# Performance work log

Hardware: AMD Instinct MI355X
Metric: run time of the kernel (lower is better)

The kernel has to match this reference:

```python
import jax, jax.numpy as jnp
import numpy as np

B, S, D = 2, 2048, 2048
H, HKV = 32, 8
HD = D // H  # 64
NEG_INF = -1e9


def _rope_tables(seq_len, head_dim):
    inv_freq = 1.0 / (10000.0 ** (np.arange(0, head_dim, 2, dtype=np.float32) / head_dim))
    t = np.arange(seq_len, dtype=np.float32)
    freqs = np.outer(t, inv_freq)                      # (S, HD/2)
    emb = np.concatenate([freqs, freqs], axis=-1)      # (S, HD)
    cos = np.cos(emb)[None, None]                      # (1,1,S,HD)
    sin = np.sin(emb)[None, None]
    return jnp.asarray(cos), jnp.asarray(sin)


def setup_inputs() -> dict:
    key = jax.random.key(0)
    ks = jax.random.split(key, 5)
    hidden_states = jax.random.normal(ks[0], (B, S, D), dtype=jnp.float32)
    # causal additive mask: 0 where allowed, -inf (large negative) where masked
    causal = jnp.tril(jnp.ones((S, S), dtype=jnp.bool_))
    attention_mask = jnp.where(causal, 0.0, NEG_INF).astype(jnp.float32)
    attention_mask = jnp.broadcast_to(attention_mask[None, None], (B, 1, S, S))
    cos, sin = _rope_tables(S, HD)
    sc = 0.02
    Wq = jax.random.normal(ks[1], (D, H * HD), dtype=jnp.float32) * sc
    Wk = jax.random.normal(ks[2], (D, HKV * HD), dtype=jnp.float32) * sc
    Wv = jax.random.normal(ks[3], (D, HKV * HD), dtype=jnp.float32) * sc
    Wo = jax.random.normal(ks[4], (H * HD, D), dtype=jnp.float32) * sc
    return {"hidden_states": hidden_states, "attention_mask": attention_mask,
            "cos": cos, "sin": sin, "Wq": Wq, "Wk": Wk, "Wv": Wv, "Wo": Wo}


def _rotate_half(x):
    x1, x2 = jnp.split(x, 2, axis=-1)
    return jnp.concatenate([-x2, x1], axis=-1)


def _apply_rope(x, cos, sin):
    # x: (B, h, S, HD); cos/sin: (1,1,S,HD)
    return x * cos + _rotate_half(x) * sin


def reference(hidden_states, attention_mask, cos, sin, Wq, Wk, Wv, Wo):
    b, s, _ = hidden_states.shape
    scale = 1.0 / np.sqrt(HD)
    q = (hidden_states @ Wq).reshape(b, s, H, HD).transpose(0, 2, 1, 3)    # (B,H,S,HD)
    k = (hidden_states @ Wk).reshape(b, s, HKV, HD).transpose(0, 2, 1, 3)  # (B,HKV,S,HD)
    v = (hidden_states @ Wv).reshape(b, s, HKV, HD).transpose(0, 2, 1, 3)
    q = _apply_rope(q, cos, sin)
    k = _apply_rope(k, cos, sin)
    # GQA: group query heads per kv head without materializing repeated KV
    g = H // HKV
    qg = q.reshape(b, HKV, g, s, HD)
    scores = jnp.einsum('bkgqd,bksd->bkgqs', qg, k) * scale               # (B,HKV,g,S,S)
    scores = scores + attention_mask[:, :, None]                          # broadcast (B,1,1,S,S)
    attn = jax.nn.softmax(scores, axis=-1)
    out = jnp.einsum('bkgqs,bksd->bkgqd', attn, v)                        # (B,HKV,g,S,HD)
    out = out.reshape(b, H, s, HD).transpose(0, 2, 1, 3).reshape(b, s, H * HD)
    return out @ Wo
```

## Files before the change

kernel.cpp:

```cpp
#include <hip/hip_runtime.h>
#include <math.h>

typedef _Float16 half8 __attribute__((ext_vector_type(8)));
typedef _Float16 half4 __attribute__((ext_vector_type(4)));
typedef _Float16 half2 __attribute__((ext_vector_type(2)));
typedef float f32x4 __attribute__((ext_vector_type(4)));

#define S_LEN 2048
#define DM    2048
#define NH    32
#define NKV   8

#define QSCALE 0.1803368801111204f
#define NSHIFT -11.541560327111707f

#if __has_builtin(__builtin_amdgcn_exp2f)
#define EXP2(x) __builtin_amdgcn_exp2f(x)
#else
#define EXP2(x) __builtin_exp2f(x)
#endif

__device__ __forceinline__ half2 pkrtz(float a, float b) {
    return __builtin_bit_cast(half2, __builtin_amdgcn_cvt_pkrtz(a, b));
}

__device__ __forceinline__ void async16(const void* g, void* l) {
    __builtin_amdgcn_global_load_lds(
        (const __attribute__((address_space(1))) unsigned int*)g,
        (__attribute__((address_space(3))) unsigned int*)l, 16, 0, 0);
}

__global__ __launch_bounds__(256) void cast_h(const float* __restrict__ x,
                                              _Float16* __restrict__ y, int n)
{
    int i = (blockIdx.x * 256 + threadIdx.x) * 4;
    if (i >= n) return;
    float4 v = *(const float4*)(x + i);
    half4 o = {(_Float16)v.x, (_Float16)v.y, (_Float16)v.z, (_Float16)v.w};
    *(half4*)(y + i) = o;
}

__global__ __launch_bounds__(256) void transpose_all(
    const float* __restrict__ Wq, const float* __restrict__ Wk,
    const float* __restrict__ Wv, const float* __restrict__ Wo,
    _Float16* __restrict__ Wqkv_t, _Float16* __restrict__ Wo_t)
{
    const int z = blockIdx.z;
    const float* W; _Float16* Wt; int N;
    if (z == 0)      { W = Wq; Wt = Wqkv_t;                        N = 2048; }
    else if (z == 1) { W = Wk; Wt = Wqkv_t + (size_t)2048 * 2048;  N = 512;  }
    else if (z == 2) { W = Wv; Wt = Wqkv_t + (size_t)2560 * 2048;  N = 512;  }
    else             { W = Wo; Wt = Wo_t;                          N = 2048; }
    if ((int)blockIdx.x * 32 >= N) return;

    __shared__ float t[32][33];
    const int n0 = blockIdx.x * 32, k0 = blockIdx.y * 32;
    const int tx = threadIdx.x & 31, ty = threadIdx.x >> 5;
#pragma unroll
    for (int i = 0; i < 32; i += 8)
        t[ty + i][tx] = W[(size_t)(k0 + ty + i) * N + n0 + tx];
    __syncthreads();
#pragma unroll
    for (int i = 0; i < 32; i += 8)
        Wt[(size_t)(n0 + ty + i) * 2048 + k0 + tx] = (_Float16)t[tx][ty + i];
}

__global__ __launch_bounds__(512, 2) void gemm_h(
    const _Float16* __restrict__ A, const _Float16* __restrict__ Bt,
    void* __restrict__ Cout, int N, int K, int mode,
    const float* __restrict__ cosT, const float* __restrict__ sinT)
{
    __shared__ __align__(16) _Float16 Lds[2][4][8192];
    const int tid  = threadIdx.x;
    const int lane = tid & 63;
    const int wave = tid >> 6;
    const int lm = lane & 15, quad = lane >> 4;
    const int wm = wave >> 2;
    const int wn = wave & 3;

    const int gx  = gridDim.x;
    const int nwg = gx * gridDim.y;
    const int lin = blockIdx.y * gx + blockIdx.x;
    const int tsw = (lin & 7) * (nwg >> 3) + (lin >> 3);
    const int bm  = (tsw / gx) * 256, bn = (tsw % gx) * 256;
    const int nt  = K >> 6;

    const int sr   = tid >> 3;
    const int lg   = (tid & 7) ^ (sr & 7);
    const int grow = sr * 2 + (lg >> 2);
    const int gcol = (lg & 3) << 3;
    const _Float16* pA0 = A  + (size_t)(bm + grow) * K + gcol;
    const _Float16* pB0 = Bt + (size_t)(bn + grow) * K + gcol;
    char* ldsb = (char*)Lds + tid * 16;

#define STAGE(t, idx) do { if ((t) < nt) {                          \
        const int koff_ = (t) * 64 + (((idx) >> 1) << 5);           \
        const _Float16* s_ = (((idx) & 1) ? pA0 : pB0) + koff_;     \
        char* d_ = ldsb + (((t) & 1) << 16) + ((idx) << 14);        \
        async16(s_, d_);                                            \
        async16(s_ + (size_t)128 * K, d_ + 8192);                   \
    } } while (0)

    const int chsw = (((((lm & 1) << 2) | quad) ^ (lm >> 1)) << 3);
    const int ar = (wm << 6) + (lm >> 1);
    const int br = (wn << 5) + (lm >> 1);
    const _Float16* Lh = (const _Float16*)Lds;

    f32x4 acc[8][4];
#pragma unroll
    for (int i = 0; i < 8; ++i)
#pragma unroll
        for (int j = 0; j < 4; ++j) acc[i][j] = (f32x4){0.f, 0.f, 0.f, 0.f};

    STAGE(0, 0); STAGE(0, 1); STAGE(0, 2); STAGE(0, 3);
    STAGE(1, 0); STAGE(1, 1); STAGE(1, 2);
    if (nt > 1) asm volatile("s_waitcnt vmcnt(6)" ::: "memory");
    else        asm volatile("s_waitcnt vmcnt(0)" ::: "memory");
    __builtin_amdgcn_s_barrier();

    half8 af[4], bf[4];
#define MFMA16(mb)                                                            \
    _Pragma("unroll") for (int i_ = 0; i_ < 4; ++i_)                          \
    _Pragma("unroll") for (int j_ = 0; j_ < 4; ++j_)                          \
        acc[(mb) + i_][j_] = __builtin_amdgcn_mfma_f32_16x16x32_f16(          \
            af[i_], bf[j_], acc[(mb) + i_][j_], 0, 0, 0);

#define PH_BAR()  __builtin_amdgcn_s_barrier();                               \
                  asm volatile("s_waitcnt lgkmcnt(0)" ::: "memory");          \
                  __builtin_amdgcn_s_setprio(1)
#define PH_END()  __builtin_amdgcn_s_setprio(0);                              \
                  __builtin_amdgcn_s_barrier()

    int p = 0;
    for (int G = 0; G < nt; ++G, p ^= 1) {
        const _Float16* Lp = Lh + (p << 15);
        const _Float16* Au0 = Lp + 8192  + ar * 64 + chsw;
        const _Float16* Au1 = Lp + 24576 + ar * 64 + chsw;
        const _Float16* Bu0 = Lp +         br * 64 + chsw;
        const _Float16* Bu1 = Lp + 16384 + br * 64 + chsw;
#pragma unroll
        for (int i = 0; i < 4; ++i) af[i] = *(const half8*)(Au0 + i * 512);
#pragma unroll
        for (int j = 0; j < 4; ++j) bf[j] = *(const half8*)(Bu0 + j * 512);
        STAGE(G + 1, 3);
        PH_BAR(); MFMA16(0); PH_END();
#pragma unroll
        for (int i = 0; i < 4; ++i) af[i] = *(const half8*)(Au0 + 2048 + i * 512);
        STAGE(G + 2, 0);
        PH_BAR(); MFMA16(4); PH_END();
#pragma unroll
        for (int i = 0; i < 4; ++i) af[i] = *(const half8*)(Au1 + i * 512);
#pragma unroll
        for (int j = 0; j < 4; ++j) bf[j] = *(const half8*)(Bu1 + j * 512);
        STAGE(G + 2, 1);
        PH_BAR(); MFMA16(0); PH_END();
#pragma unroll
        for (int i = 0; i < 4; ++i) af[i] = *(const half8*)(Au1 + 2048 + i * 512);
        STAGE(G + 2, 2);
        PH_BAR(); MFMA16(4);
        __builtin_amdgcn_s_setprio(0);
        if (G + 2 < nt) asm volatile("s_waitcnt vmcnt(6)" ::: "memory");
        else            asm volatile("s_waitcnt vmcnt(0)" ::: "memory");
        __builtin_amdgcn_s_barrier();
    }
#undef STAGE
#undef MFMA16
#undef PH_BAR
#undef PH_END

    const int mrowq = bm + (wm << 7) + (quad << 2);
    if (mode == 0) {
        float* C = (float*)Cout;
        const int col0 = bn + (wn << 6) + lm;
#pragma unroll
        for (int mf = 0; mf < 8; ++mf)
#pragma unroll
            for (int r = 0; r < 4; ++r) {
                const int m = mrowq + mf * 16 + r;
#pragma unroll
                for (int nf = 0; nf < 4; ++nf)
                    C[(size_t)m * N + col0 + nf * 16] = acc[mf][nf][r];
            }
        return;
    }

    _Float16* Cq = (_Float16*)Cout;
    _Float16* Ck = Cq + (size_t)2 * NH * S_LEN * 64;
    _Float16* Cv = Ck + (size_t)2 * NKV * S_LEN * 64;
    const int colbase = bn + (wn << 6);
    const int region = (colbase >= 2560) ? 2 : (colbase >= 2048) ? 1 : 0;

    if (region == 2) {
        const int head = (colbase - 2560) >> 6;
#pragma unroll
        for (int mf = 0; mf < 8; ++mf) {
            const int m0 = mrowq + mf * 16;
            const int b = m0 >> 11, s0 = m0 & 2047;
#pragma unroll
            for (int nf = 0; nf < 4; ++nf) {
                half2 lo = pkrtz(acc[mf][nf][0], acc[mf][nf][1]);
                half2 hi = pkrtz(acc[mf][nf][2], acc[mf][nf][3]);
                half4 ov = {lo[0], lo[1], hi[0], hi[1]};
                *(half4*)(Cv + ((((size_t)b * NKV + head) << 6) + lm + nf * 16) * S_LEN + s0) = ov;
            }
        }
        return;
    }

    const float qscale = (region == 0) ? QSCALE : 1.0f;
    const int head = (region == 0) ? (colbase >> 6) : ((colbase - 2048) >> 6);
    _Float16* Cdst = (region == 0) ? Cq : Ck;
    const int nh = (region == 0) ? NH : NKV;
#pragma unroll
    for (int mf = 0; mf < 8; ++mf)
#pragma unroll
        for (int r = 0; r < 4; ++r) {
            int m = mrowq + mf * 16 + r;
            int b = m >> 11, s = m & 2047;
            const float c0 = cosT[s * 64 + lm], c16 = cosT[s * 64 + lm + 16];
            const float s0 = sinT[s * 64 + lm], s16 = sinT[s * 64 + lm + 16];
            float a0r = acc[mf][0][r], a1r = acc[mf][1][r];
            float a2r = acc[mf][2][r], a3r = acc[mf][3][r];
            float o0 = (a0r * c0  - a2r * s0)  * qscale;
            float o1 = (a1r * c16 - a3r * s16) * qscale;
            float o2 = (a2r * c0  + a0r * s0)  * qscale;
            float o3 = (a3r * c16 + a1r * s16) * qscale;
            _Float16* d = Cdst + ((((size_t)b * nh + head) * S_LEN + s) << 6) + lm;
            d[0]  = (_Float16)o0;
            d[16] = (_Float16)o1;
            d[32] = (_Float16)o2;
            d[48] = (_Float16)o3;
        }
}

#define LSWOFS(row, halfofs) \
    ((row) * 64 + (((((halfofs) >> 3) & 7) ^ ((row) & 7)) << 3) + ((halfofs) & 7))

__global__ __launch_bounds__(256, 2) void attn_h(
    const _Float16* __restrict__ q, const _Float16* __restrict__ k,
    const _Float16* __restrict__ vt, _Float16* __restrict__ x2)
{
    __shared__ __align__(16) _Float16 Ks[2][64 * 64];
    __shared__ __align__(16) _Float16 Vts[2][64 * 64];

    const int kvh = blockIdx.y, b = blockIdx.z;
    const int tid = threadIdx.x;
    const int wave = tid >> 6, lane = tid & 63;
    const int lm = lane & 15, quad = lane >> 4;
    const int h = kvh * 4 + wave;

    const int qtT[2] = {63 - (int)blockIdx.x, (int)blockIdx.x};
    const int ktm[2] = {(qtT[0] * 32 + 31) >> 6, (qtT[1] * 32 + 31) >> 6};

    const _Float16* kbase  = k  + ((((size_t)b * NKV + kvh) * S_LEN) << 6);
    const _Float16* vtbase = vt + ((((size_t)b * NKV + kvh) << 6) * S_LEN);

    half8 qf[2][2][2];
#pragma unroll
    for (int tp = 0; tp < 2; ++tp) {
        const _Float16* qb = q + ((((size_t)b * NH + h) * S_LEN + qtT[tp] * 32) << 6);
#pragma unroll
        for (int i = 0; i < 2; ++i)
#pragma unroll
            for (int kk = 0; kk < 2; ++kk)
                qf[tp][i][kk] = *(const half8*)(qb + (i * 16 + lm) * 64 + kk * 32 + quad * 8);
    }

    f32x4 accOT[2][2][4];
    float lpart[2][2];
#pragma unroll
    for (int tp = 0; tp < 2; ++tp)
#pragma unroll
        for (int i = 0; i < 2; ++i) {
            lpart[tp][i] = 0.f;
#pragma unroll
            for (int j = 0; j < 4; ++j) accOT[tp][i][j] = (f32x4){0.f, 0.f, 0.f, 0.f};
        }

    const int f0 = tid * 16, f1 = 4096 + tid * 16;
    const int r0 = f0 >> 7, r1 = f1 >> 7;
    const int c0 = ((f0 >> 4) & 7) ^ (r0 & 7);
    const int c1 = ((f1 >> 4) & 7) ^ (r1 & 7);
    const char* ksrc0 = (const char*)kbase  + r0 * 128 + c0 * 16;
    const char* ksrc1 = (const char*)kbase  + r1 * 128 + c1 * 16;
    const char* vsrc0 = (const char*)vtbase + (size_t)r0 * 4096 + c0 * 16;
    const char* vsrc1 = (const char*)vtbase + (size_t)r1 * 4096 + c1 * 16;

#define STAGEKV(kt, nb) do {                                          \
        async16(ksrc0 + (size_t)(kt) * 8192, (char*)Ks[nb]  + f0);    \
        async16(ksrc1 + (size_t)(kt) * 8192, (char*)Ks[nb]  + f1);    \
        async16(vsrc0 + (kt) * 128,          (char*)Vts[nb] + f0);    \
        async16(vsrc1 + (kt) * 128,          (char*)Vts[nb] + f1);    \
    } while (0)

    STAGEKV(0, 0);
    asm volatile("s_waitcnt vmcnt(0)" ::: "memory");
    __builtin_amdgcn_s_barrier();

    for (int kt = 0; kt <= ktm[0]; ++kt) {
        const int cur = kt & 1;
        if (kt < ktm[0]) STAGEKV(kt + 1, cur ^ 1);
        const _Float16* Kc = Ks[cur];
        const _Float16* Vc = Vts[cur];

        half8 kf[4][2];
        half4 vtf[4][4];
#pragma unroll
        for (int t = 0; t < 4; ++t) {
#pragma unroll
            for (int kk = 0; kk < 2; ++kk)
                kf[t][kk] = *(const half8*)(Kc + LSWOFS(t * 16 + lm, kk * 32 + quad * 8));
#pragma unroll
            for (int j = 0; j < 4; ++j)
                vtf[j][t] = *(const half4*)(Vc + LSWOFS(j * 16 + lm, t * 16 + quad * 4));
        }

#pragma unroll
        for (int tp = 0; tp < 2; ++tp) {
            if (kt > ktm[tp]) continue;
            const bool diag = (kt == ktm[tp]);
#pragma unroll
            for (int i = 0; i < 2; ++i) {
                f32x4 sc[4];
                __builtin_amdgcn_s_setprio(1);
#pragma unroll
                for (int t = 0; t < 4; ++t) {
                    f32x4 z = (f32x4){NSHIFT, NSHIFT, NSHIFT, NSHIFT};
                    z = __builtin_amdgcn_mfma_f32_16x16x32_f16(kf[t][0], qf[tp][i][0], z, 0, 0, 0);
                    z = __builtin_amdgcn_mfma_f32_16x16x32_f16(kf[t][1], qf[tp][i][1], z, 0, 0, 0);
                    sc[t] = z;
                }
                __builtin_amdgcn_s_setprio(0);
                if (diag) {
                    const int qpos = qtT[tp] * 32 + i * 16 + lm;
#pragma unroll
                    for (int t = 0; t < 4; ++t)
#pragma unroll
                        for (int r = 0; r < 4; ++r) {
                            int key = kt * 64 + t * 16 + quad * 4 + r;
                            if (key > qpos) sc[t][r] = -30000.f;
                        }
                }
                half4 pt[4];
                float lp = 0.f;
#pragma unroll
                for (int t = 0; t < 4; ++t) {
                    float p0 = EXP2(sc[t][0]), p1 = EXP2(sc[t][1]);
                    float p2 = EXP2(sc[t][2]), p3 = EXP2(sc[t][3]);
                    lp += (p0 + p1) + (p2 + p3);
                    half2 lo = pkrtz(p0, p1);
                    half2 hi = pkrtz(p2, p3);
                    pt[t] = (half4){lo[0], lo[1], hi[0], hi[1]};
                }
                lpart[tp][i] += lp;
                __builtin_amdgcn_s_setprio(1);
#pragma unroll
                for (int j = 0; j < 4; ++j)
#pragma unroll
                    for (int t = 0; t < 4; ++t)
                        accOT[tp][i][j] = __builtin_amdgcn_mfma_f32_16x16x16f16(
                            vtf[j][t], pt[t], accOT[tp][i][j], 0, 0, 0);
                __builtin_amdgcn_s_setprio(0);
            }
        }
        asm volatile("s_waitcnt vmcnt(0)" ::: "memory");
        __builtin_amdgcn_s_barrier();
    }
#undef STAGEKV

#pragma unroll
    for (int tp = 0; tp < 2; ++tp)
#pragma unroll
        for (int i = 0; i < 2; ++i) {
            float l = lpart[tp][i];
            l += __shfl_xor(l, 16);
            l += __shfl_xor(l, 32);
            const float inv = 1.f / l;
            const size_t row = (size_t)b * S_LEN + qtT[tp] * 32 + i * 16 + lm;
#pragma unroll
            for (int j = 0; j < 4; ++j) {
                f32x4 o = accOT[tp][i][j];
                half2 lo = pkrtz(o[0] * inv, o[1] * inv);
                half2 hi = pkrtz(o[2] * inv, o[3] * inv);
                half4 ov = {lo[0], lo[1], hi[0], hi[1]};
                *(half4*)(x2 + row * DM + h * 64 + j * 16 + quad * 4) = ov;
            }
        }
}

extern "C" void kernel_launch(void* const* d_in, const int* in_sizes, int n_in,
                              void* d_out, int out_size, void* d_ws, size_t ws_size,
                              hipStream_t stream)
{
    const float* hidden = (const float*)d_in[0];
    const float* cosT = (const float*)d_in[2];
    const float* sinT = (const float*)d_in[3];
    const float* Wq = (const float*)d_in[4];
    const float* Wk = (const float*)d_in[5];
    const float* Wv = (const float*)d_in[6];
    const float* Wo = (const float*)d_in[7];
    float* out = (float*)d_out;

    _Float16* w = (_Float16*)d_ws;
    _Float16* hid_h  = w;  w += (size_t)4096 * 2048;
    _Float16* Wqkv_t = w;  w += (size_t)3072 * 2048;
    _Float16* Wo_t   = w;  w += (size_t)2048 * 2048;
    _Float16* qh     = w;  w += (size_t)2 * NH * S_LEN * 64;
    _Float16* kh     = w;  w += (size_t)2 * NKV * S_LEN * 64;
    _Float16* vth    = w;  w += (size_t)2 * NKV * S_LEN * 64;
    _Float16* x2h    = w;

    dim3 blk(256);
    cast_h<<<dim3(8192), blk, 0, stream>>>(hidden, hid_h, 8388608);
    transpose_all<<<dim3(64, 64, 4), blk, 0, stream>>>(Wq, Wk, Wv, Wo, Wqkv_t, Wo_t);

    gemm_h<<<dim3(12, 16), dim3(512), 0, stream>>>(hid_h, Wqkv_t, qh, 3072, 2048, 1, cosT, sinT);

    attn_h<<<dim3(32, 8, 2), blk, 0, stream>>>(qh, kh, vth, x2h);

    gemm_h<<<dim3(8, 16), dim3(512), 0, stream>>>(x2h, Wo_t, out, 2048, 2048, 0, nullptr, nullptr);
}
```

Measured before the change: 323.1 us.

## Merge input cast into transpose kernel and restructure GEMM pipeline into two half-phases

Folds the hidden-state fp32-to-fp16 cast into the weight transpose kernel as an extra grid z-slice, removing one kernel launch. The GEMM main loop changes from four quarter-phases with a two-tile prefetch to two half-phases that each load eight A fragments and issue 32 MFMAs, prefetching only one tile ahead. This cuts the barrier count per K-step but shortens the lookahead on global loads and raises register pressure from the larger A fragment array.

```diff
diff --git a/kernel.cpp b/kernel.cpp
--- a/kernel.cpp
+++ b/kernel.cpp
@@ -30,22 +30,23 @@
         (__attribute__((address_space(3))) unsigned int*)l, 16, 0, 0);
 }
 
-__global__ __launch_bounds__(256) void cast_h(const float* __restrict__ x,
-                                              _Float16* __restrict__ y, int n)
-{
-    int i = (blockIdx.x * 256 + threadIdx.x) * 4;
-    if (i >= n) return;
-    float4 v = *(const float4*)(x + i);
-    half4 o = {(_Float16)v.x, (_Float16)v.y, (_Float16)v.z, (_Float16)v.w};
-    *(half4*)(y + i) = o;
-}
-
-__global__ __launch_bounds__(256) void transpose_all(
+__global__ __launch_bounds__(256) void prep_all(
     const float* __restrict__ Wq, const float* __restrict__ Wk,
     const float* __restrict__ Wv, const float* __restrict__ Wo,
-    _Float16* __restrict__ Wqkv_t, _Float16* __restrict__ Wo_t)
+    const float* __restrict__ hidden,
+    _Float16* __restrict__ Wqkv_t, _Float16* __restrict__ Wo_t,
+    _Float16* __restrict__ hid_h)
 {
     const int z = blockIdx.z;
+    if (z == 4) {
+        const size_t i = ((size_t)(blockIdx.y * 64 + blockIdx.x) * 256 + threadIdx.x) * 8;
+        float4 v0 = *(const float4*)(hidden + i);
+        float4 v1 = *(const float4*)(hidden + i + 4);
+        half8 o = {(_Float16)v0.x, (_Float16)v0.y, (_Float16)v0.z, (_Float16)v0.w,
+                   (_Float16)v1.x, (_Float16)v1.y, (_Float16)v1.z, (_Float16)v1.w};
+        *(half8*)(hid_h + i) = o;
+        return;
+    }
     const float* W; _Float16* Wt; int N;
     if (z == 0)      { W = Wq; Wt = Wqkv_t;                        N = 2048; }
     else if (z == 1) { W = Wk; Wt = Wqkv_t + (size_t)2048 * 2048;  N = 512;  }
@@ -113,23 +114,22 @@
         for (int j = 0; j < 4; ++j) acc[i][j] = (f32x4){0.f, 0.f, 0.f, 0.f};
 
     STAGE(0, 0); STAGE(0, 1); STAGE(0, 2); STAGE(0, 3);
-    STAGE(1, 0); STAGE(1, 1); STAGE(1, 2);
-    if (nt > 1) asm volatile("s_waitcnt vmcnt(6)" ::: "memory");
+    if (nt > 1) asm volatile("s_waitcnt vmcnt(4)" ::: "memory");
     else        asm volatile("s_waitcnt vmcnt(0)" ::: "memory");
     __builtin_amdgcn_s_barrier();
 
-    half8 af[4], bf[4];
-#define MFMA16(mb)                                                            \
-    _Pragma("unroll") for (int i_ = 0; i_ < 4; ++i_)                          \
+    half8 af[8], bf[4];
+#define MFMA32()                                                              \
+    _Pragma("unroll") for (int i_ = 0; i_ < 8; ++i_)                          \
     _Pragma("unroll") for (int j_ = 0; j_ < 4; ++j_)                          \
-        acc[(mb) + i_][j_] = __builtin_amdgcn_mfma_f32_16x16x32_f16(          \
-            af[i_], bf[j_], acc[(mb) + i_][j_], 0, 0, 0);
-
-#define PH_BAR()  __builtin_amdgcn_s_barrier();                               \
-                  asm volatile("s_waitcnt lgkmcnt(0)" ::: "memory");          \
-                  __builtin_amdgcn_s_setprio(1)
-#define PH_END()  __builtin_amdgcn_s_setprio(0);                              \
-                  __builtin_amdgcn_s_barrier()
+        acc[i_][j_] = __builtin_amdgcn_mfma_f32_16x16x32_f16(                 \
+            af[i_], bf[j_], acc[i_][j_], 0, 0, 0);
+
+#define PH_TAIL(cond)                                                         \
+    __builtin_amdgcn_s_setprio(0);                                            \
+    if (cond) asm volatile("s_waitcnt vmcnt(4)" ::: "memory");                \
+    else      asm volatile("s_waitcnt vmcnt(0)" ::: "memory");                \
+    __builtin_amdgcn_s_barrier()
 
     int p = 0;
     for (int G = 0; G < nt; ++G, p ^= 1) {
@@ -138,35 +138,27 @@
         const _Float16* Au1 = Lp + 24576 + ar * 64 + chsw;
         const _Float16* Bu0 = Lp +         br * 64 + chsw;
         const _Float16* Bu1 = Lp + 16384 + br * 64 + chsw;
-#pragma unroll
-        for (int i = 0; i < 4; ++i) af[i] = *(const half8*)(Au0 + i * 512);
+        const bool more = (G + 1) < nt;
+#pragma unroll
+        for (int i = 0; i < 8; ++i) af[i] = *(const half8*)(Au0 + i * 512);
 #pragma unroll
         for (int j = 0; j < 4; ++j) bf[j] = *(const half8*)(Bu0 + j * 512);
-        STAGE(G + 1, 3);
-        PH_BAR(); MFMA16(0); PH_END();
-#pragma unroll
-        for (int i = 0; i < 4; ++i) af[i] = *(const half8*)(Au0 + 2048 + i * 512);
-        STAGE(G + 2, 0);
-        PH_BAR(); MFMA16(4); PH_END();
-#pragma unroll
-        for (int i = 0; i < 4; ++i) af[i] = *(const half8*)(Au1 + i * 512);
+        STAGE(G + 1, 0); STAGE(G + 1, 1);
+        __builtin_amdgcn_s_setprio(1);
+        MFMA32();
+        PH_TAIL(more);
+#pragma unroll
+        for (int i = 0; i < 8; ++i) af[i] = *(const half8*)(Au1 + i * 512);
 #pragma unroll
         for (int j = 0; j < 4; ++j) bf[j] = *(const half8*)(Bu1 + j * 512);
-        STAGE(G + 2, 1);
-        PH_BAR(); MFMA16(0); PH_END();
-#pragma unroll
-        for (int i = 0; i < 4; ++i) af[i] = *(const half8*)(Au1 + 2048 + i * 512);
-        STAGE(G + 2, 2);
-        PH_BAR(); MFMA16(4);
-        __builtin_amdgcn_s_setprio(0);
-        if (G + 2 < nt) asm volatile("s_waitcnt vmcnt(6)" ::: "memory");
-        else            asm volatile("s_waitcnt vmcnt(0)" ::: "memory");
-        __builtin_amdgcn_s_barrier();
+        STAGE(G + 1, 2); STAGE(G + 1, 3);
+        __builtin_amdgcn_s_setprio(1);
+        MFMA32();
+        PH_TAIL(more);
     }
 #undef STAGE
-#undef MFMA16
-#undef PH_BAR
-#undef PH_END
+#undef MFMA32
+#undef PH_TAIL
 
     const int mrowq = bm + (wm << 7) + (quad << 2);
     if (mode == 0) {
@@ -411,8 +403,8 @@
     _Float16* x2h    = w;
 
     dim3 blk(256);
-    cast_h<<<dim3(8192), blk, 0, stream>>>(hidden, hid_h, 8388608);
-    transpose_all<<<dim3(64, 64, 4), blk, 0, stream>>>(Wq, Wk, Wv, Wo, Wqkv_t, Wo_t);
+    prep_all<<<dim3(64, 64, 5), blk, 0, stream>>>(Wq, Wk, Wv, Wo, hidden,
+                                                  Wqkv_t, Wo_t, hid_h);
 
     gemm_h<<<dim3(12, 16), dim3(512), 0, stream>>>(hid_h, Wqkv_t, qh, 3072, 2048, 1, cosT, sinT);
 
```

New measurement: 307.9 us. -4.7%, faster.
